# Kernel optimization log

Measured on AMD Instinct MI355X. Metric: run time of the kernel, lower is better.

The kernel has to match this reference:

```python
import jax, jax.numpy as jnp
import numpy as np

# Static config (matches init_kwargs)
DIM, HEADS = 192, 6
PL, LAT, LON = 8, 96, 180
WP, WL, WW = 2, 6, 12          # window size (pressure, lat, lon)
SP, SL, SW = 1, 3, 6           # shift size
N = WP * WL * WW               # tokens per window = 144
NPL, NLAT, NLON = PL // WP, LAT // WL, LON // WW   # 4, 16, 15
NW = NPL * NLAT                # type_of_windows = 64 (lat/pl-dependent bias)
HD = DIM // HEADS              # 32
L = PL * LAT * LON
BIAS_LEN = (2 * WW - 1) * WL * WL * WP * WP   # 3312
EPS = 1e-5


def _position_index():
    # Earth-specific relative position index (Pangu): absolute-position
    # dependence along pressure and latitude, relative along longitude.
    zi = np.arange(WP); zj = -np.arange(WP) * WP
    hi = np.arange(WL); hj = -np.arange(WL) * WL
    w = np.arange(WW)
    c1 = np.stack(np.meshgrid(zi, hi, w, indexing='ij')).reshape(3, -1)
    c2 = np.stack(np.meshgrid(zj, hj, w, indexing='ij')).reshape(3, -1)
    c = (c1[:, :, None] - c2[:, None, :]).transpose(1, 2, 0).copy()
    c[:, :, 2] += WW - 1
    c[:, :, 1] *= 2 * WW - 1
    c[:, :, 0] *= (2 * WW - 1) * WL * WL
    return c.sum(-1)  # (N, N) in [0, BIAS_LEN)


def _attn_mask():
    # Shifted-window mask: lon is periodic on the globe (roll only), so
    # masking is applied along pressure and latitude boundaries only.
    img = np.zeros((1, PL, LAT, LON, 1), np.float32)
    cnt = 0
    for pl in (slice(0, -WP), slice(-WP, -SP), slice(-SP, None)):
        for la in (slice(0, -WL), slice(-WL, -SL), slice(-SL, None)):
            img[:, pl, la, :, :] = cnt
            cnt += 1
    mw = img.reshape(1, NPL, WP, NLAT, WL, NLON, WW, 1)
    mw = mw.transpose(0, 5, 1, 3, 2, 4, 6, 7).reshape(NLON, NW, N)
    am = mw[:, :, None, :] - mw[:, :, :, None]
    return np.where(am != 0, -100.0, 0.0).astype(np.float32)  # (NLON, NW, N, N)


POS_IDX = jnp.asarray(_position_index())
ATTN_MASK = jnp.asarray(_attn_mask())


def layer_norm(x, g, b):
    m = x.mean(-1, keepdims=True)
    v = ((x - m) ** 2).mean(-1, keepdims=True)
    return (x - m) * jax.lax.rsqrt(v + EPS) * g + b


def setup_inputs() -> dict:
    key = jax.random.key(0)
    ks = jax.random.split(key, 10)
    s = 0.02
    return {
        'x': jax.random.normal(ks[0], (1, L, DIM), jnp.float32),
        'norm1_g': jnp.ones((DIM,), jnp.float32),
        'norm1_b': jnp.zeros((DIM,), jnp.float32),
        'qkv_w': jax.random.normal(ks[1], (DIM, 3 * DIM), jnp.float32) * s,
        'qkv_b': jnp.zeros((3 * DIM,), jnp.float32),
        'earth_bias': jax.random.normal(ks[2], (BIAS_LEN, NW, HEADS), jnp.float32) * s,
        'proj_w': jax.random.normal(ks[3], (DIM, DIM), jnp.float32) * s,
        'proj_b': jnp.zeros((DIM,), jnp.float32),
        'norm2_g': jnp.ones((DIM,), jnp.float32),
        'norm2_b': jnp.zeros((DIM,), jnp.float32),
        'fc1_w': jax.random.normal(ks[4], (DIM, 4 * DIM), jnp.float32) * s,
        'fc1_b': jnp.zeros((4 * DIM,), jnp.float32),
        'fc2_w': jax.random.normal(ks[5], (4 * DIM, DIM), jnp.float32) * s,
        'fc2_b': jnp.zeros((DIM,), jnp.float32),
    }


def reference(x, norm1_g, norm1_b, qkv_w, qkv_b, earth_bias, proj_w, proj_b,
              norm2_g, norm2_b, fc1_w, fc1_b, fc2_w, fc2_b):
    B, Ltok, C = x.shape
    shortcut = x
    h = layer_norm(x, norm1_g, norm1_b).reshape(B, PL, LAT, LON, C)
    # shifted windows (lon is periodic -> plain roll)
    h = jnp.roll(h, shift=(-SP, -SL, -SW), axis=(1, 2, 3))
    # window partition -> (B*NLON, NW, N, C); lon windows folded into batch
    xw = h.reshape(B, NPL, WP, NLAT, WL, NLON, WW, C)
    xw = xw.transpose(0, 5, 1, 3, 2, 4, 6, 7).reshape(B * NLON, NW, N, C)
    # earth-specific attention
    qkv = (xw @ qkv_w + qkv_b).reshape(B * NLON, NW, N, 3, HEADS, HD)
    qkv = qkv.transpose(3, 0, 1, 4, 2, 5)  # (3, B_, NW, H, N, HD)
    q, k, v = qkv[0], qkv[1], qkv[2]
    attn = jnp.einsum('bwhnd,bwhmd->bwhnm', q * (HD ** -0.5), k)
    bias = earth_bias[POS_IDX].reshape(N, N, NW, HEADS).transpose(2, 3, 0, 1)
    attn = attn + bias[None]                        # (B_, NW, H, N, N)
    attn = attn.reshape(B, NLON, NW, HEADS, N, N) + ATTN_MASK[None, :, :, None]
    attn = jax.nn.softmax(attn.reshape(B * NLON, NW, HEADS, N, N), axis=-1)
    out = jnp.einsum('bwhnm,bwhmd->bwhnd', attn, v)
    out = out.transpose(0, 1, 3, 2, 4).reshape(B * NLON, NW, N, C)
    out = out @ proj_w + proj_b
    # window reverse + roll back
    h = out.reshape(B, NLON, NPL, NLAT, WP, WL, WW, C)
    h = h.transpose(0, 2, 4, 3, 5, 1, 6, 7).reshape(B, PL, LAT, LON, C)
    h = jnp.roll(h, shift=(SP, SL, SW), axis=(1, 2, 3)).reshape(B, Ltok, C)
    x = shortcut + h
    # MLP block (GELU exact, as nn.GELU default)
    y = layer_norm(x, norm2_g, norm2_b)
    y = jax.nn.gelu(y @ fc1_w + fc1_b, approximate=False) @ fc2_w + fc2_b
    return x + y
```

## Files before the change

kernel.cpp:

```cpp
#include <hip/hip_runtime.h>
#include <hip/hip_bf16.h>
#include <math.h>

typedef unsigned short u16;
typedef __attribute__((ext_vector_type(8))) short short8;
typedef __attribute__((ext_vector_type(4))) short short4v;
typedef __attribute__((ext_vector_type(4))) float f32x4;

#define MFMA(a,b,c) __builtin_amdgcn_mfma_f32_16x16x32_bf16(a,b,c,0,0,0)
#define DIM 192

__device__ __forceinline__ float bf2f(u16 u){ unsigned v=((unsigned)u)<<16; float f; __builtin_memcpy(&f,&v,4); return f; }
__device__ __forceinline__ u16 f2bf(float f){ unsigned v; __builtin_memcpy(&v,&f,4); v = v + 0x7fffu + ((v>>16)&1u); return (u16)(v>>16); }

__device__ __forceinline__ void gl_lds16(const u16* g, u16* l){
  __builtin_amdgcn_global_load_lds((const __attribute__((address_space(1))) unsigned int*)g,
                                   (__attribute__((address_space(3))) unsigned int*)l, 16, 0, 0);
}

__device__ __forceinline__ int win_to_tok(int r){
  int lon = r/9216; int rem = r - lon*9216;
  int w = rem/144, n = rem - w*144;
  int ip=w>>4, il=w&15;
  int wp=n/72, t=n-wp*72, wl=t/12, ww=t-wl*12;
  int p=ip*2+wp, la=il*6+wl, lo=lon*12+ww;
  int p0=p+1;  if(p0>=8)   p0-=8;
  int la0=la+3; if(la0>=96) la0-=96;
  int lo0=lo+6; if(lo0>=180)lo0-=180;
  return (p0*96+la0)*180+lo0;
}

__global__ __launch_bounds__(256) void ln1_window_kernel(
    const float* __restrict__ x, const float* __restrict__ g, const float* __restrict__ b,
    u16* __restrict__ A)
{
  int r = blockIdx.x*4 + (threadIdx.x>>6);
  int lane = threadIdx.x & 63;
  size_t src = (size_t)win_to_tok(r)*DIM;
  float v0=x[src+lane], v1=x[src+64+lane], v2=x[src+128+lane];
  float s=v0+v1+v2;
  for(int m=32;m>=1;m>>=1) s += __shfl_xor(s,m);
  float mean = s*(1.f/192.f);
  float d0=v0-mean,d1=v1-mean,d2=v2-mean;
  float q=d0*d0+d1*d1+d2*d2;
  for(int m=32;m>=1;m>>=1) q += __shfl_xor(q,m);
  float rstd = rsqrtf(q*(1.f/192.f)+1e-5f);
  size_t o = (size_t)r*DIM;
  A[o+lane]     = f2bf(d0*rstd*g[lane]     + b[lane]);
  A[o+64+lane]  = f2bf(d1*rstd*g[64+lane]  + b[64+lane]);
  A[o+128+lane] = f2bf(d2*rstd*g[128+lane] + b[128+lane]);
}

__global__ __launch_bounds__(256) void transpose_bf16_kernel(
    const float* __restrict__ src, u16* __restrict__ dst, int K, int N)
{
  int idx = blockIdx.x*256 + threadIdx.x;
  if (idx >= K*N) return;
  int k = idx / N, n = idx - k*N;
  dst[n*K + k] = f2bf(src[idx]);
}

__global__ __launch_bounds__(256) void pf_w1_kernel(const float* __restrict__ fc1w, u16* __restrict__ W1f){
  int idx = blockIdx.x*256 + threadIdx.x;
  int e = idx & 7, g3 = idx >> 3;
  int g = g3 % 24, r3 = g3 / 24;
  int r = r3 & 63, ch = r3 >> 6;
  int k = ((g ^ (r&7))<<3) + e;
  W1f[idx] = f2bf(fc1w[(size_t)k*768 + ch*64 + r]);
}
__global__ __launch_bounds__(256) void pf_w2_kernel(const float* __restrict__ fc2w, u16* __restrict__ W2f){
  int idx = blockIdx.x*256 + threadIdx.x;
  int e = idx & 7, g3 = idx >> 3;
  int g = g3 & 7, r3 = g3 >> 3;
  int r = r3 % 192, ch = r3 / 192;
  int k = ch*64 + ((g ^ (r&7))<<3) + e;
  W2f[idx] = f2bf(fc2w[(size_t)k*192 + r]);
}

__global__ __launch_bounds__(256) void bias_expand_kernel(
    const float* __restrict__ eb, u16* __restrict__ B2)
{
  __shared__ int t1s[144], t2s[144], rgs[144];
  __shared__ float ebs[3312];
  int bid = blockIdx.x;
  int w = bid / 6;
  int tid = threadIdx.x;
  if (tid < 144) {
    int n = tid;
    int wp=n/72, t=n-wp*72, wl=t/12, ww=t-wl*12;
    t1s[n] = wp*828 + wl*23 + ww;
    t2s[n] = 1656*wp + 138*wl - ww + 11;
    int ip = w>>4, il = w&15;
    int p = ip*2+wp, la = il*6+wl;
    int rp = (p<6)?0:((p<7)?1:2);
    int rl = (la<90)?0:((la<93)?1:2);
    rgs[n] = rp*3+rl;
  }
  for (int i = tid; i < 3312; i += 256) ebs[i] = eb[(size_t)i*384 + bid];
  __syncthreads();
  size_t ob = (size_t)bid*20736;
  for (int idx = tid; idx < 20736; idx += 256) {
    int i = idx & 3, lane = (idx>>2)&63, t = idx>>8;
    int mt = t%9, nt = t/9;
    int n = nt*16 + (lane&15);
    int m = mt*16 + ((lane>>4)<<2) + i;
    float bv = ebs[t1s[n]+t2s[m]];
    bv += (rgs[n]==rgs[m]) ? 0.f : -100.f;
    B2[ob + idx] = f2bf(bv);
  }
}

#define SM_WS   0
#define SM_QS   38400
#define SM_KS   49920
#define SM_VS   61440
#define SM_PS   72192
#define SMEM3   120576

__global__ __launch_bounds__(576) void attn_kernel(
    const u16* __restrict__ A,
    const u16* __restrict__ Wt,
    const float* __restrict__ qkvb,
    const u16* __restrict__ Bexp,
    u16* __restrict__ O)
{
  extern __shared__ char smem[];
  u16* Ws = (u16*)(smem + SM_WS);
  u16* qs = (u16*)(smem + SM_QS);
  u16* ks_= (u16*)(smem + SM_KS);
  u16* vs = (u16*)(smem + SM_VS);
  u16* Ps = (u16*)(smem + SM_PS);

  int bid = blockIdx.x;
  int logical = (bid & 7)*720 + (bid >> 3);
  int lon = logical % 15;
  int wh  = logical / 15;
  int h = wh % 6, w = wh / 6;
  int tid = threadIdx.x, lane = tid & 63, wv = tid >> 6;

  {
    int rr = tid % 96, chunk = tid / 96;
    int mat = rr >> 5, c = rr & 31;
    const u16* s = Wt + (size_t)(mat*192 + h*32 + c)*192 + chunk*32;
    u16* d = Ws + rr*200 + chunk*32;
    *(uint4*)(d)    = *(const uint4*)(s);
    *(uint4*)(d+8)  = *(const uint4*)(s+8);
    *(uint4*)(d+16) = *(const uint4*)(s+16);
    *(uint4*)(d+24) = *(const uint4*)(s+24);
  }
  if (tid < 512) { int c = tid>>4; vs[c*168 + 144 + (tid&15)] = 0; }
  for (int j=0;j<4;j++){ int idx = tid + j*576; int row = idx>>4;
    if (row < 144) Ps[row*168 + 144 + (idx&15)] = 0; }
  __syncthreads();

  size_t winbase = (size_t)(lon*64 + w)*144;
  int r0 = wv*16;
  int l15 = lane & 15, lg = lane >> 4;

  short8 af[6];
  {
    const u16* arow = A + (winbase + r0 + l15)*DIM + 8*lg;
    #pragma unroll
    for (int k0=0;k0<6;k0++) af[k0] = *(const short8*)(arow + k0*32);
  }
  const float qscale = 0.17677669529663687f;

  #pragma unroll
  for (int mt=0; mt<2; mt++) {
    f32x4 acc = {0.f,0.f,0.f,0.f};
    const u16* wrow = Ws + (mt*16 + l15)*200 + 8*lg;
    #pragma unroll
    for (int k0=0;k0<6;k0++) acc = MFMA(*(const short8*)(wrow + k0*32), af[k0], acc);
    short4v pk;
    #pragma unroll
    for (int i=0;i<4;i++) pk[i] = (short)f2bf((acc[i] + qkvb[h*32 + mt*16 + 4*lg + i])*qscale);
    *(short4v*)(qs + (r0 + l15)*40 + mt*16 + 4*lg) = pk;
  }
  #pragma unroll
  for (int mt=0; mt<2; mt++) {
    f32x4 acc = {0.f,0.f,0.f,0.f};
    const u16* wrow = Ws + (32 + mt*16 + l15)*200 + 8*lg;
    #pragma unroll
    for (int k0=0;k0<6;k0++) acc = MFMA(*(const short8*)(wrow + k0*32), af[k0], acc);
    short4v pk;
    #pragma unroll
    for (int i=0;i<4;i++) pk[i] = (short)f2bf(acc[i] + qkvb[192 + h*32 + mt*16 + 4*lg + i]);
    *(short4v*)(ks_ + (r0 + l15)*40 + mt*16 + 4*lg) = pk;
  }
  #pragma unroll
  for (int ct=0; ct<2; ct++) {
    f32x4 acc = {0.f,0.f,0.f,0.f};
    const u16* wrow = Ws + (64 + ct*16 + l15)*200 + 8*lg;
    #pragma unroll
    for (int k0=0;k0<6;k0++) acc = MFMA(af[k0], *(const short8*)(wrow + k0*32), acc);
    float bias = qkvb[384 + h*32 + ct*16 + l15];
    short4v pk;
    #pragma unroll
    for (int i=0;i<4;i++) pk[i] = (short)f2bf(acc[i] + bias);
    *(short4v*)(vs + (ct*16 + l15)*168 + r0 + 4*lg) = pk;
  }
  __syncthreads();

  short8 bq = *(const short8*)(qs + (r0 + l15)*40 + 8*lg);
  f32x4 sa[9];
  #pragma unroll
  for (int mt=0; mt<9; mt++) {
    f32x4 z = {0.f,0.f,0.f,0.f};
    sa[mt] = MFMA(*(const short8*)(ks_ + (mt*16 + l15)*40 + 8*lg), bq, z);
  }
  {
    const u16* bb = Bexp + (((size_t)wh*9 + wv)*9)*256 + lane*4;
    #pragma unroll
    for (int mt=0; mt<9; mt++) {
      short4v pk = *(const short4v*)(bb + mt*256);
      #pragma unroll
      for (int i=0;i<4;i++) sa[mt][i] += bf2f((u16)pk[i]);
    }
  }
  float rsum = 0.f;
  #pragma unroll
  for (int mt=0; mt<9; mt++)
    #pragma unroll
    for (int i=0;i<4;i++) { float e = __expf(sa[mt][i]); sa[mt][i] = e; rsum += e; }
  rsum += __shfl_xor(rsum, 16);
  rsum += __shfl_xor(rsum, 32);
  float rinv = 1.f / rsum;
  #pragma unroll
  for (int mt=0; mt<9; mt++) {
    short4v pk;
    #pragma unroll
    for (int i=0;i<4;i++) pk[i] = (short)f2bf(sa[mt][i]);
    *(short4v*)(Ps + (r0 + l15)*168 + mt*16 + 4*lg) = pk;
  }

  #pragma unroll
  for (int ct2=0; ct2<2; ct2++) {
    f32x4 acc = {0.f,0.f,0.f,0.f};
    const u16* vr = vs + (ct2*16 + l15)*168 + 8*lg;
    const u16* pr = Ps + (r0 + l15)*168 + 8*lg;
    #pragma unroll
    for (int k0=0;k0<5;k0++) acc = MFMA(*(const short8*)(vr + 32*k0), *(const short8*)(pr + 32*k0), acc);
    short4v pk;
    #pragma unroll
    for (int i=0;i<4;i++) pk[i] = (short)f2bf(acc[i]*rinv);
    *(short4v*)(O + (winbase + r0 + l15)*DIM + h*32 + ct2*16 + 4*lg) = pk;
  }
}

#define SMEMP (73728 + 512)
__global__ __launch_bounds__(512, 4) void proj_ln2_kernel(
    const u16* __restrict__ AT,
    const u16* __restrict__ Pw,
    const float* __restrict__ pb, const float* __restrict__ x,
    const float* __restrict__ n2g, const float* __restrict__ n2b,
    float* __restrict__ out, u16* __restrict__ Y)
{
  extern __shared__ char smem[];
  u16* Pws = (u16*)smem;
  int* tokmap = (int*)(smem + 73728);
  int tid = threadIdx.x;
  size_t rbase = (size_t)blockIdx.x*128;
  #pragma unroll
  for (int j=0;j<9;j++){
    int g = j*512 + tid;
    int row = g/24, jj = g - row*24;
    uint4 t = *(const uint4*)(Pw + (size_t)row*192 + jj*8);
    *(uint4*)(Pws + row*192 + ((jj ^ (row&7))*8)) = t;
  }
  if (tid < 128) tokmap[tid] = win_to_tok((int)rbase + tid);
  __syncthreads();

  int lane = tid&63, wv = tid>>6, r0 = wv*16;
  int l15 = lane&15, lg = lane>>4;
  short8 af[6];
  const u16* arow = AT + (rbase + r0 + l15)*DIM + 8*lg;
  #pragma unroll
  for (int k0=0;k0<6;k0++) af[k0] = *(const short8*)(arow + k0*32);

  f32x4 acc[12];
  #pragma unroll
  for (int ct=0; ct<12; ct++) {
    f32x4 a = {0.f,0.f,0.f,0.f};
    const u16* wr = Pws + (ct*16+l15)*192;
    #pragma unroll
    for (int k0=0;k0<6;k0++) a = MFMA(af[k0], *(const short8*)(wr + (((k0*4+lg)^(l15&7))*8)), a);
    acc[ct] = a;
  }
  int toks[4];
  #pragma unroll
  for (int i=0;i<4;i++) toks[i] = tokmap[r0 + 4*lg + i];
  #pragma unroll
  for (int ct=0; ct<12; ct++) {
    int col = ct*16+l15;
    float bias = pb[col];
    #pragma unroll
    for (int i=0;i<4;i++){
      size_t o = (size_t)toks[i]*DIM + col;
      float v = x[o] + acc[ct][i] + bias;
      out[o] = v;
      acc[ct][i] = v;
    }
  }
  float s[4] = {0,0,0,0};
  #pragma unroll
  for (int ct=0; ct<12; ct++) for (int i=0;i<4;i++) s[i] += acc[ct][i];
  #pragma unroll
  for (int i=0;i<4;i++){ for (int m=1;m<16;m<<=1) s[i] += __shfl_xor(s[i], m, 16); s[i] *= (1.f/192.f); }
  float q[4] = {0,0,0,0};
  #pragma unroll
  for (int ct=0; ct<12; ct++) for (int i=0;i<4;i++){ float d = acc[ct][i]-s[i]; q[i] += d*d; }
  #pragma unroll
  for (int i=0;i<4;i++){ for (int m=1;m<16;m<<=1) q[i] += __shfl_xor(q[i], m, 16); q[i] = rsqrtf(q[i]*(1.f/192.f)+1e-5f); }
  #pragma unroll
  for (int ct=0; ct<12; ct++) {
    int col = ct*16+l15;
    float gg = n2g[col], bb = n2b[col];
    #pragma unroll
    for (int i=0;i<4;i++)
      Y[(size_t)toks[i]*DIM + col] = f2bf((acc[ct][i]-s[i])*q[i]*gg + bb);
  }
}

#define SMEM5 86016
__global__ __launch_bounds__(1024, 4) void mlp_kernel(
    const u16* __restrict__ Y,
    const u16* __restrict__ W1f,
    const float* __restrict__ b1,
    const u16* __restrict__ W2f,
    const float* __restrict__ b2,
    float* __restrict__ out)
{
  extern __shared__ char smem[];
  u16* B0 = (u16*)smem;
  u16* B1 = (u16*)(smem + 24576);
  u16* Hs = (u16*)(smem + 49152);
  int tid = threadIdx.x;
  size_t rbase = (size_t)blockIdx.x*256;
  int lane = tid&63, wv = tid>>6, r0 = wv*16;
  int l15 = lane&15, lg = lane>>4;

  short8 af[6];
  {
    const u16* yrow = Y + (rbase + r0 + l15)*DIM + 8*lg;
    #pragma unroll
    for (int k0=0;k0<6;k0++) af[k0] = *(const short8*)(yrow + k0*32);
  }

  gl_lds16(W1f + (size_t)tid*8, B0 + tid*8);
  if (tid < 512) gl_lds16(W1f + (size_t)(1024+tid)*8, B0 + (1024+tid)*8);
  __syncthreads();

  f32x4 acc2[12];
  #pragma unroll
  for (int i=0;i<12;i++) acc2[i] = (f32x4){0.f,0.f,0.f,0.f};

  const float GA = -1.5957691216057307f;
  const float GB = -0.07135481627272283f;

  for (int ch=0; ch<12; ch++) {
    {
      const u16* s2 = W2f + (size_t)ch*12288;
      gl_lds16(s2 + (size_t)tid*8, B1 + tid*8);
      if (tid < 512) gl_lds16(s2 + (size_t)(1024+tid)*8, B1 + (1024+tid)*8);
    }
    #pragma unroll
    for (int ct=0; ct<4; ct++) {
      f32x4 a1 = {0.f,0.f,0.f,0.f};
      const u16* wr = B0 + (ct*16+l15)*192;
      #pragma unroll
      for (int k0=0;k0<6;k0++) a1 = MFMA(af[k0], *(const short8*)(wr + (((k0*4+lg)^(l15&7))*8)), a1);
      float bb = b1[ch*64 + ct*16 + l15];
      #pragma unroll
      for (int i=0;i<4;i++){
        float v = a1[i] + bb;
        float t = v*v;
        float m = fmaf(t, GB, GA);
        float e = __expf(v*m);
        float hgl = v*__builtin_amdgcn_rcpf(1.f + e);
        Hs[(r0 + 4*lg + i)*72 + ct*16 + l15] = f2bf(hgl);
      }
    }
    __syncthreads();

    if (ch < 11) {
      const u16* s1 = W1f + (size_t)(ch+1)*12288;
      gl_lds16(s1 + (size_t)tid*8, B0 + tid*8);
      if (tid < 512) gl_lds16(s1 + (size_t)(1024+tid)*8, B0 + (1024+tid)*8);
    }
    #pragma unroll
    for (int k2=0; k2<2; k2++) {
      short8 ah = *(const short8*)(Hs + (r0+l15)*72 + k2*32 + 8*lg);
      #pragma unroll
      for (int ct2=0; ct2<12; ct2++) {
        const u16* wr2 = B1 + (ct2*16+l15)*64 + (((k2*4+lg)^(l15&7))*8);
        acc2[ct2] = MFMA(ah, *(const short8*)(wr2), acc2[ct2]);
      }
    }
    __syncthreads();
  }
  #pragma unroll
  for (int ct2=0; ct2<12; ct2++) {
    int col = ct2*16+l15;
    float bb = b2[col];
    #pragma unroll
    for (int i=0;i<4;i++){
      size_t o = (rbase + r0 + 4*lg + i)*DIM + col;
      out[o] = out[o] + acc2[ct2][i] + bb;
    }
  }
}

extern "C" void kernel_launch(void* const* d_in, const int* in_sizes, int n_in,
                              void* d_out, int out_size, void* d_ws, size_t ws_size,
                              hipStream_t stream) {
  const float* x    = (const float*)d_in[0];
  const float* n1g  = (const float*)d_in[1];
  const float* n1b  = (const float*)d_in[2];
  const float* qkvw = (const float*)d_in[3];
  const float* qkvb = (const float*)d_in[4];
  const float* eb   = (const float*)d_in[5];
  const float* projw= (const float*)d_in[6];
  const float* projb= (const float*)d_in[7];
  const float* n2g  = (const float*)d_in[8];
  const float* n2b  = (const float*)d_in[9];
  const float* fc1w = (const float*)d_in[10];
  const float* fc1b = (const float*)d_in[11];
  const float* fc2w = (const float*)d_in[12];
  const float* fc2b = (const float*)d_in[13];
  float* out = (float*)d_out;
  char* ws = (char*)d_ws;

  u16* A   = (u16*)(ws);
  u16* AT  = (u16*)(ws + 53084160);
  u16* Wq  = (u16*)(ws + 106168320);
  u16* Pw  = (u16*)(ws + 106389504);
  u16* W1f = (u16*)(ws + 106463232);
  u16* W2f = (u16*)(ws + 106758144);
  u16* Bexp = (u16*)d_out;

  hipFuncSetAttribute((const void*)attn_kernel,     hipFuncAttributeMaxDynamicSharedMemorySize, SMEM3);
  hipFuncSetAttribute((const void*)proj_ln2_kernel, hipFuncAttributeMaxDynamicSharedMemorySize, SMEMP);
  hipFuncSetAttribute((const void*)mlp_kernel,      hipFuncAttributeMaxDynamicSharedMemorySize, SMEM5);

  transpose_bf16_kernel<<<432, 256, 0, stream>>>(qkvw, Wq, 192, 576);
  transpose_bf16_kernel<<<144, 256, 0, stream>>>(projw, Pw, 192, 192);
  pf_w1_kernel<<<576, 256, 0, stream>>>(fc1w, W1f);
  pf_w2_kernel<<<576, 256, 0, stream>>>(fc2w, W2f);
  bias_expand_kernel<<<384, 256, 0, stream>>>(eb, Bexp);
  ln1_window_kernel<<<34560, 256, 0, stream>>>(x, n1g, n1b, A);
  attn_kernel<<<5760, 576, SMEM3, stream>>>(A, Wq, qkvb, Bexp, AT);
  proj_ln2_kernel<<<1080, 512, SMEMP, stream>>>(AT, Pw, projb, x, n2g, n2b, out, A);
  mlp_kernel<<<540, 1024, SMEM5, stream>>>(A, W1f, fc1b, W2f, fc2b, out);
}
```

Before: 491.5 us.

## Restructure MLP kernel into 32-wide hidden chunks with double-buffered weights

The MLP kernel now handles 128 rows per block with 512 threads, so the grid grows from 540 to 1080 blocks. It walks the hidden dimension in 24 chunks of 32 instead of 12 chunks of 64. W1 and W2 chunks are double-buffered in LDS and prefetched two chunks ahead, which cuts the barriers per iteration from two to one and overlaps the loads with the MFMA work. The weight pre-swizzle kernels are changed to match the new 32-wide layout. In exchange there are more loop iterations, a shorter K per MFMA batch, and more weight traffic in total because each block now covers fewer rows.

After: 469.0 us. 1.05x faster.

```diff
diff --git a/kernel.cpp b/kernel.cpp
--- a/kernel.cpp
+++ b/kernel.cpp
@@ -64,16 +64,16 @@
   int idx = blockIdx.x*256 + threadIdx.x;
   int e = idx & 7, g3 = idx >> 3;
   int g = g3 % 24, r3 = g3 / 24;
-  int r = r3 & 63, ch = r3 >> 6;
+  int r = r3 & 31, hc = r3 >> 5;
   int k = ((g ^ (r&7))<<3) + e;
-  W1f[idx] = f2bf(fc1w[(size_t)k*768 + ch*64 + r]);
+  W1f[idx] = f2bf(fc1w[(size_t)k*768 + hc*32 + r]);
 }
 __global__ __launch_bounds__(256) void pf_w2_kernel(const float* __restrict__ fc2w, u16* __restrict__ W2f){
   int idx = blockIdx.x*256 + threadIdx.x;
   int e = idx & 7, g3 = idx >> 3;
-  int g = g3 & 7, r3 = g3 >> 3;
-  int r = r3 % 192, ch = r3 / 192;
-  int k = ch*64 + ((g ^ (r&7))<<3) + e;
+  int g = g3 & 3, r3 = g3 >> 2;
+  int r = r3 % 192, hc = r3 / 192;
+  int k = hc*32 + ((g ^ (r&3))<<3) + e;
   W2f[idx] = f2bf(fc2w[(size_t)k*192 + r]);
 }
 
@@ -321,8 +321,8 @@
   }
 }
 
-#define SMEM5 86016
-__global__ __launch_bounds__(1024, 4) void mlp_kernel(
+#define SMEM5 59392
+__global__ __launch_bounds__(512, 4) void mlp_kernel(
     const u16* __restrict__ Y,
     const u16* __restrict__ W1f,
     const float* __restrict__ b1,
@@ -331,11 +331,13 @@
     float* __restrict__ out)
 {
   extern __shared__ char smem[];
-  u16* B0 = (u16*)smem;
-  u16* B1 = (u16*)(smem + 24576);
-  u16* Hs = (u16*)(smem + 49152);
+  u16* W1b0 = (u16*)smem;
+  u16* W1b1 = (u16*)(smem + 12288);
+  u16* W2b0 = (u16*)(smem + 24576);
+  u16* W2b1 = (u16*)(smem + 36864);
+  u16* Hs   = (u16*)(smem + 49152);
   int tid = threadIdx.x;
-  size_t rbase = (size_t)blockIdx.x*256;
+  size_t rbase = (size_t)blockIdx.x*128;
   int lane = tid&63, wv = tid>>6, r0 = wv*16;
   int l15 = lane&15, lg = lane>>4;
 
@@ -346,8 +348,17 @@
     for (int k0=0;k0<6;k0++) af[k0] = *(const short8*)(yrow + k0*32);
   }
 
-  gl_lds16(W1f + (size_t)tid*8, B0 + tid*8);
-  if (tid < 512) gl_lds16(W1f + (size_t)(1024+tid)*8, B0 + (1024+tid)*8);
+  {
+    gl_lds16(W1f + (size_t)tid*8, W1b0 + tid*8);
+    if (tid < 256) gl_lds16(W1f + (size_t)(512+tid)*8, W1b0 + (512+tid)*8);
+    gl_lds16(W2f + (size_t)tid*8, W2b0 + tid*8);
+    if (tid < 256) gl_lds16(W2f + (size_t)(512+tid)*8, W2b0 + (512+tid)*8);
+    const u16* s1 = W1f + 6144; const u16* s2 = W2f + 6144;
+    gl_lds16(s1 + (size_t)tid*8, W1b1 + tid*8);
+    if (tid < 256) gl_lds16(s1 + (size_t)(512+tid)*8, W1b1 + (512+tid)*8);
+    gl_lds16(s2 + (size_t)tid*8, W2b1 + tid*8);
+    if (tid < 256) gl_lds16(s2 + (size_t)(512+tid)*8, W2b1 + (512+tid)*8);
+  }
   __syncthreads();
 
   f32x4 acc2[12];
@@ -357,19 +368,16 @@
   const float GA = -1.5957691216057307f;
   const float GB = -0.07135481627272283f;
 
-  for (int ch=0; ch<12; ch++) {
-    {
-      const u16* s2 = W2f + (size_t)ch*12288;
-      gl_lds16(s2 + (size_t)tid*8, B1 + tid*8);
-      if (tid < 512) gl_lds16(s2 + (size_t)(1024+tid)*8, B1 + (1024+tid)*8);
-    }
-    #pragma unroll
-    for (int ct=0; ct<4; ct++) {
+  for (int hc=0; hc<24; hc++) {
+    u16* B1w = (hc&1) ? W1b1 : W1b0;
+    u16* B2w = (hc&1) ? W2b1 : W2b0;
+    #pragma unroll
+    for (int ct=0; ct<2; ct++) {
       f32x4 a1 = {0.f,0.f,0.f,0.f};
-      const u16* wr = B0 + (ct*16+l15)*192;
+      const u16* wr = B1w + (ct*16+l15)*192;
       #pragma unroll
       for (int k0=0;k0<6;k0++) a1 = MFMA(af[k0], *(const short8*)(wr + (((k0*4+lg)^(l15&7))*8)), a1);
-      float bb = b1[ch*64 + ct*16 + l15];
+      float bb = b1[hc*32 + ct*16 + l15];
       #pragma unroll
       for (int i=0;i<4;i++){
         float v = a1[i] + bb;
@@ -377,26 +385,28 @@
         float m = fmaf(t, GB, GA);
         float e = __expf(v*m);
         float hgl = v*__builtin_amdgcn_rcpf(1.f + e);
-        Hs[(r0 + 4*lg + i)*72 + ct*16 + l15] = f2bf(hgl);
+        Hs[(r0 + 4*lg + i)*40 + ct*16 + l15] = f2bf(hgl);
       }
     }
-    __syncthreads();
-
-    if (ch < 11) {
-      const u16* s1 = W1f + (size_t)(ch+1)*12288;
-      gl_lds16(s1 + (size_t)tid*8, B0 + tid*8);
-      if (tid < 512) gl_lds16(s1 + (size_t)(1024+tid)*8, B0 + (1024+tid)*8);
-    }
-    #pragma unroll
-    for (int k2=0; k2<2; k2++) {
-      short8 ah = *(const short8*)(Hs + (r0+l15)*72 + k2*32 + 8*lg);
+    {
+      short8 ah = *(const short8*)(Hs + (r0+l15)*40 + 8*lg);
       #pragma unroll
       for (int ct2=0; ct2<12; ct2++) {
-        const u16* wr2 = B1 + (ct2*16+l15)*64 + (((k2*4+lg)^(l15&7))*8);
+        const u16* wr2 = B2w + (ct2*16+l15)*32 + ((lg ^ (l15&3))*8);
         acc2[ct2] = MFMA(ah, *(const short8*)(wr2), acc2[ct2]);
       }
     }
     __syncthreads();
+    if (hc < 22) {
+      const u16* s1 = W1f + (size_t)(hc+2)*6144;
+      const u16* s2 = W2f + (size_t)(hc+2)*6144;
+      u16* d1 = (hc&1) ? W1b1 : W1b0;
+      u16* d2 = (hc&1) ? W2b1 : W2b0;
+      gl_lds16(s1 + (size_t)tid*8, d1 + tid*8);
+      if (tid < 256) gl_lds16(s1 + (size_t)(512+tid)*8, d1 + (512+tid)*8);
+      gl_lds16(s2 + (size_t)tid*8, d2 + tid*8);
+      if (tid < 256) gl_lds16(s2 + (size_t)(512+tid)*8, d2 + (512+tid)*8);
+    }
   }
   #pragma unroll
   for (int ct2=0; ct2<12; ct2++) {
@@ -450,5 +460,5 @@
   ln1_window_kernel<<<34560, 256, 0, stream>>>(x, n1g, n1b, A);
   attn_kernel<<<5760, 576, SMEM3, stream>>>(A, Wq, qkvb, Bexp, AT);
   proj_ln2_kernel<<<1080, 512, SMEMP, stream>>>(AT, Pw, projb, x, n2g, n2b, out, A);
-  mlp_kernel<<<540, 1024, SMEM5, stream>>>(A, W1f, fc1b, W2f, fc2b, out);
-}
+  mlp_kernel<<<1080, 512, SMEM5, stream>>>(A, W1f, fc1b, W2f, fc2b, out);
+}
```
